# Performance work log

Hardware: AMD Instinct MI355X
Metric: run time of the kernel (lower is better)

## Reference

```python
import jax, jax.numpy as jnp
import numpy as np
from jax import lax

OBS_LEN = 8
PRED_LEN = 12
BATCH = 131072
EMB = 128
HID = 128


def _lstm_cell(h, c, x, Wih, Whh, b):
    # PyTorch LSTM gate order: i, f, g, o
    z = x @ Wih + h @ Whh + b  # (B, 4H)
    i, f, g, o = jnp.split(z, 4, axis=-1)
    c_new = jax.nn.sigmoid(f) * c + jax.nn.sigmoid(i) * jnp.tanh(g)
    h_new = jax.nn.sigmoid(o) * jnp.tanh(c_new)
    return h_new, c_new


def setup_inputs() -> dict:
    key = jax.random.key(0)
    ks = jax.random.split(key, 8)
    p = lambda k, s: jax.random.normal(k, s, dtype=jnp.float32) * 0.1
    return {
        "obs_traj": jax.random.normal(ks[0], (OBS_LEN, BATCH, 2), dtype=jnp.float32),
        # encoder input embedding (Linear 2 -> EMB)
        "We": p(ks[1], (2, EMB)), "be": jnp.zeros((EMB,), jnp.float32),
        # encoder LSTM
        "Wih_e": p(ks[2], (EMB, 4 * HID)), "Whh_e": p(ks[3], (HID, 4 * HID)),
        "b_e": jnp.zeros((4 * HID,), jnp.float32),
        # decoder input embedding (Linear 2 -> EMB)
        "Wd": p(ks[4], (2, EMB)), "bd": jnp.zeros((EMB,), jnp.float32),
        # decoder LSTM
        "Wih_d": p(ks[5], (EMB, 4 * HID)), "Whh_d": p(ks[6], (HID, 4 * HID)),
        "b_d": jnp.zeros((4 * HID,), jnp.float32),
        # hidden2pos (Linear HID -> 2)
        "Wo": p(ks[7], (HID, 2)), "bo": jnp.zeros((2,), jnp.float32),
        "pred_len": PRED_LEN,
    }


def reference(obs_traj, We, be, Wih_e, Whh_e, b_e, Wd, bd, Wih_d, Whh_d, b_d, Wo, bo, pred_len):
    B = obs_traj.shape[1]
    H = Whh_e.shape[0]
    dt = obs_traj.dtype

    # ---- Encoder: embed positions, run LSTM over obs_len ----
    emb = obs_traj @ We + be  # (obs_len, B, EMB)
    h0 = jnp.zeros((B, H), dt)
    c0 = jnp.zeros((B, H), dt)

    def enc_step(carry, x_t):
        h, c = carry
        h, c = _lstm_cell(h, c, x_t, Wih_e, Whh_e, b_e)
        return (h, c), None

    (h_enc, _), _ = lax.scan(enc_step, (h0, c0), emb)

    # ---- Decoder: state = (h_final, zeros); first pos directly from h_final ----
    pos0 = h_enc @ Wo + bo  # (B, 2)
    h_d = h_enc
    c_d = jnp.zeros_like(h_enc)

    def dec_step(carry, _):
        h, c, pos = carry
        x = pos @ Wd + bd  # embed previous predicted position
        h, c = _lstm_cell(h, c, x, Wih_d, Whh_d, b_d)
        pos_new = h @ Wo + bo
        return (h, c, pos_new), pos_new

    _, rest = lax.scan(dec_step, (h_d, c_d, pos0), None, length=pred_len - 1)
    pred_traj = jnp.concatenate([pos0[None], rest], axis=0)  # (pred_len, B, 2)
    return pred_traj
```

## Files before the change

### kernel.cpp

```cpp
#include <hip/hip_runtime.h>


#define OBS_LEN 8
#define PRED_LEN 12
#define BATCH 131072
#define HID 128
#define NZ 512
#define KWT 128
#define XK 32
#define A2S 40

typedef float f32x4 __attribute__((ext_vector_type(4)));
typedef float f32x2 __attribute__((ext_vector_type(2)));
typedef unsigned short u16x8 __attribute__((ext_vector_type(8)));
typedef __bf16 bf16x8 __attribute__((ext_vector_type(8)));

#define K2F 1.4426950408889634f

static __device__ __forceinline__ unsigned short cvt1(float f) {
  __bf16 b = (__bf16)f;
  return __builtin_bit_cast(unsigned short, b);
}
static __device__ __forceinline__ float bf2f(unsigned short h) {
  return __uint_as_float(((unsigned int)h) << 16);
}

__global__ void prep_weights(const float* __restrict__ We,   const float* __restrict__ be,
                             const float* __restrict__ Wih_e,const float* __restrict__ Whh_e,
                             const float* __restrict__ b_e,
                             const float* __restrict__ Wd,   const float* __restrict__ bd,
                             const float* __restrict__ Wih_d,const float* __restrict__ Whh_d,
                             const float* __restrict__ b_d,
                             const float* __restrict__ Wo,   const float* __restrict__ bo,
                             unsigned short* __restrict__ wt_enc,
                             unsigned short* __restrict__ wt_dec,
                             unsigned short* __restrict__ xw_enc,
                             unsigned short* __restrict__ xw_dec) {
  const int c = blockIdx.x & (NZ - 1);
  const bool dec = blockIdx.x >= NZ;
  const int cg = c >> 6, gate = (c >> 4) & 3, cl = c & 15;
  const int unit = cg * 16 + cl;
  const int n = gate * HID + unit;
  const float s = (gate == 2) ? (-2.f * K2F) : (-K2F);

  const float* Whh = dec ? Whh_d : Whh_e;
  const float* Wih = dec ? Wih_d : Wih_e;
  const float* Wem = dec ? Wd : We;
  const float* bem = dec ? bd : be;
  const float* bl  = dec ? b_d : b_e;
  unsigned short* wt = dec ? wt_dec : wt_enc;
  unsigned short* xw = dec ? xw_dec : xw_enc;

  float wx = 0.f, wy = 0.f;
  for (int e = 0; e < HID; ++e) {
    wx += Wem[e] * Wih[e * NZ + n];
    wy += Wem[HID + e] * Wih[e * NZ + n];
  }
  for (int k = threadIdx.x; k < KWT; k += 64) {
    float v = Whh[k * NZ + n];
    if (dec) v += Wo[k * 2] * wx + Wo[k * 2 + 1] * wy;
    wt[c * KWT + k] = cvt1(s * v);
  }
  if (threadIdx.x == 0) {
    float bb = bl[n];
    for (int e = 0; e < HID; ++e) bb += bem[e] * Wih[e * NZ + n];
    if (dec) bb += bo[0] * wx + bo[1] * wy;
    unsigned short* xr = xw + c * XK;
    for (int k = 5; k < XK; ++k) xr[k] = 0;
    if (dec) {
      xr[0] = 0; xr[1] = 0; xr[2] = cvt1(s * bb); xr[3] = 0; xr[4] = 0;
    } else {
      xr[0] = cvt1(s * wx); xr[1] = cvt1(s * wy); xr[2] = cvt1(s * bb);
      xr[3] = xr[0]; xr[4] = xr[1];
    }
  }
}


#define MFMA(A, B, C)                                                          \
  __builtin_amdgcn_mfma_f32_16x16x32_bf16(                                     \
      __builtin_bit_cast(bf16x8, (A)), __builtin_bit_cast(bf16x8, (B)), (C),   \
      0, 0, 0)

#define EXP4(D, S)                                                             \
  { f32x4 _s = (S);                                                            \
    D[0] = __builtin_amdgcn_exp2f(_s[0]); D[1] = __builtin_amdgcn_exp2f(_s[1]);\
    D[2] = __builtin_amdgcn_exp2f(_s[2]); D[3] = __builtin_amdgcn_exp2f(_s[3]); }
#define RCP4(D, S)                                                             \
  { f32x4 _r = (S);                                                            \
    D[0] = __builtin_amdgcn_rcpf(_r[0]); D[1] = __builtin_amdgcn_rcpf(_r[1]);  \
    D[2] = __builtin_amdgcn_rcpf(_r[2]); D[3] = __builtin_amdgcn_rcpf(_r[3]); }

#define LOADW(WT, XW)                                                          \
  { _Pragma("unroll")                                                          \
    for (int kc = 0; kc < 4; ++kc) {                                           \
      _Pragma("unroll")                                                        \
      for (int g = 0; g < 4; ++g)                                              \
        bfr[kc][g] =                                                           \
            *(const u16x8*)&(WT)[(cg * 64 + g * 16 + l15) * KWT + kc * 32 +    \
                                 l4 * 8];                                      \
    }                                                                          \
    _Pragma("unroll")                                                          \
    for (int g = 0; g < 4; ++g)                                                \
      xfr[g] = *(const u16x8*)&(XW)[(cg * 64 + g * 16 + l15) * XK + l4 * 8]; }

#define MMX(ACC, X)                                                            \
  { u16x8 mm_a2a = *(const u16x8*)&A2[(X)*32 * A2S + l15 * A2S + l4 * 8];      \
    u16x8 mm_a2b =                                                             \
        *(const u16x8*)&A2[(X)*32 * A2S + (16 + l15) * A2S + l4 * 8];          \
    _Pragma("unroll")                                                          \
    for (int g = 0; g < 4; ++g) {                                              \
      ACC[0][g] = MFMA(mm_a2a, xfr[g], ZROV);                                  \
      ACC[1][g] = MFMA(mm_a2b, xfr[g], ZROV);                                  \
    }                                                                          \
    _Pragma("unroll")                                                          \
    for (int kc = 0; kc < 4; ++kc) {                                           \
      const int mm_g = (((kc * 4 + l4) ^ l15) << 3);                           \
      u16x8 mm_a0 = *(const u16x8*)&hL[(X)*4096 + l15 * 128 + mm_g];           \
      u16x8 mm_a1 = *(const u16x8*)&hL[(X)*4096 + (16 + l15) * 128 + mm_g];    \
      _Pragma("unroll")                                                        \
      for (int g = 0; g < 4; ++g) {                                            \
        ACC[0][g] = MFMA(mm_a0, bfr[kc][g], ACC[0][g]);                        \
        ACC[1][g] = MFMA(mm_a1, bfr[kc][g], ACC[1][g]);                        \
      } } }

#define GATEC(ACC, CRR, X)                                                     \
  { _Pragma("unroll")                                                          \
    for (int m = 0; m < 2; ++m) {                                              \
      f32x4 g_eB, g_eA, g_eG, g_eO;                                            \
      EXP4(g_eB, ACC[m][0]) EXP4(g_eA, ACC[m][1])                              \
      EXP4(g_eG, ACC[m][2]) EXP4(g_eO, ACC[m][3])                              \
      f32x4 g_a1 = 1.f + g_eA, g_b1 = 1.f + g_eB, g_g1 = 1.f + g_eG;           \
      f32x4 g_bg = g_b1 * g_g1;                                                \
      f32x4 g_rd; RCP4(g_rd, g_a1 * g_bg)                                      \
      f32x4 g_cv = (CRR[m] * g_bg + (1.f - g_eG) * g_a1) * g_rd;               \
      CRR[m] = g_cv;                                                           \
      f32x4 g_eC; EXP4(g_eC, g_cv * (-2.f * K2F))                              \
      f32x4 g_rh; RCP4(g_rh, (1.f + g_eO) * (1.f + g_eC))                      \
      f32x4 g_hv = (1.f - g_eC) * g_rh;                                        \
      const int g_R0 = 16 * m + l4 * 4;                                        \
      _Pragma("unroll")                                                        \
      for (int r = 0; r < 4; ++r)                                              \
        hL[(X)*4096 + (g_R0 + r) * 128 +                                       \
           ((uh ^ ((g_R0 + r) & 15)) << 3) + ul] = cvt1(g_hv[r]);              \
    } }

#define POSC(S, X)                                                             \
  { const int pp_r = tid >> 4, pp_q = tid & 15;                                \
    u16x8 pp_h = *(const u16x8*)&hL[(X)*4096 + pp_r * 128 +                    \
                                    ((pp_q ^ (pp_r & 15)) << 3)];              \
    const float* pp_w = WoL + pp_q * 16;                                       \
    f32x4 pp_w0 = *(const f32x4*)pp_w;                                         \
    f32x4 pp_w1 = *(const f32x4*)(pp_w + 4);                                   \
    f32x4 pp_w2 = *(const f32x4*)(pp_w + 8);                                   \
    f32x4 pp_w3 = *(const f32x4*)(pp_w + 12);                                  \
    f32x2 pp_s = (f32x2){0.f, 0.f};                                            \
    pp_s += bf2f(pp_h[0]) * (f32x2){pp_w0[0], pp_w0[1]};                       \
    pp_s += bf2f(pp_h[1]) * (f32x2){pp_w0[2], pp_w0[3]};                       \
    pp_s += bf2f(pp_h[2]) * (f32x2){pp_w1[0], pp_w1[1]};                       \
    pp_s += bf2f(pp_h[3]) * (f32x2){pp_w1[2], pp_w1[3]};                       \
    pp_s += bf2f(pp_h[4]) * (f32x2){pp_w2[0], pp_w2[1]};                       \
    pp_s += bf2f(pp_h[5]) * (f32x2){pp_w2[2], pp_w2[3]};                       \
    pp_s += bf2f(pp_h[6]) * (f32x2){pp_w3[0], pp_w3[1]};                       \
    pp_s += bf2f(pp_h[7]) * (f32x2){pp_w3[2], pp_w3[3]};                       \
    pp_s[0] += __shfl_xor(pp_s[0], 1); pp_s[1] += __shfl_xor(pp_s[1], 1);      \
    pp_s[0] += __shfl_xor(pp_s[0], 2); pp_s[1] += __shfl_xor(pp_s[1], 2);      \
    pp_s[0] += __shfl_xor(pp_s[0], 4); pp_s[1] += __shfl_xor(pp_s[1], 4);      \
    pp_s[0] += __shfl_xor(pp_s[0], 8); pp_s[1] += __shfl_xor(pp_s[1], 8);      \
    if (pp_q == 0) {                                                           \
      float2 pp_o; pp_o.x = pp_s[0] + bo0; pp_o.y = pp_s[1] + bo1;             \
      ((float2*)out)[(size_t)(S)*BATCH + row0 + (X)*32 + pp_r] = pp_o;         \
    } }

#define STAGE_OBS_A2(T, X)                                                     \
  if (tid < 32) {                                                              \
    float2 so_p =                                                              \
        ((const float2*)obs)[(size_t)(T)*BATCH + row0 + (X)*32 + tid];         \
    unsigned short so_x = cvt1(so_p.x), so_y = cvt1(so_p.y);                   \
    unsigned short* so_r = &A2[(X)*32 * A2S + tid * A2S];                      \
    so_r[0] = so_x; so_r[1] = so_y; so_r[2] = 0x3F80u;                         \
    so_r[3] = cvt1(so_p.x - bf2f(so_x));                                       \
    so_r[4] = cvt1(so_p.y - bf2f(so_y));                                       \
  }

#define STAGE_DEC_A2(X)                                                        \
  if (tid < 32) {                                                              \
    unsigned short* sd_r = &A2[(X)*32 * A2S + tid * A2S];                      \
    sd_r[0] = 0; sd_r[1] = 0; sd_r[2] = 0x3F80u; sd_r[3] = 0; sd_r[4] = 0;     \
  }

__global__ __launch_bounds__(512, 2) void lstm_fused(
    const float* __restrict__ obs,
    const unsigned short* __restrict__ wt_enc,
    const unsigned short* __restrict__ wt_dec,
    const unsigned short* __restrict__ xw_enc,
    const unsigned short* __restrict__ xw_dec,
    const float* __restrict__ Wo, const float* __restrict__ bo,
    float* __restrict__ out) {
  __shared__ unsigned short hL[2 * 32 * 128];
  __shared__ unsigned short A2[2 * 32 * A2S];
  __shared__ float WoL[HID * 2];

  const int tid = threadIdx.x;
  const int lane = tid & 63;
  const int cg = tid >> 6;
  const int l15 = lane & 15;
  const int l4 = lane >> 4;
  const int row0 = blockIdx.x * 64;
  const int u = cg * 16 + l15, uh = u >> 3, ul = u & 7;
  const float bo0 = bo[0], bo1 = bo[1];
  const f32x4 ZROV = {0.f, 0.f, 0.f, 0.f};

  {
    u16x8 z8 = (u16x8){0, 0, 0, 0, 0, 0, 0, 0};
    *(u16x8*)&hL[tid * 8] = z8;
    *(u16x8*)&hL[4096 + tid * 8] = z8;
    unsigned short* az = &A2[tid * 5];
    az[0] = 0; az[1] = 0; az[2] = 0; az[3] = 0; az[4] = 0;
  }
  if (tid < HID) { WoL[tid * 2] = Wo[tid * 2]; WoL[tid * 2 + 1] = Wo[tid * 2 + 1]; }

  u16x8 bfr[4][4], xfr[4];
  LOADW(wt_enc, xw_enc);

  f32x4 accA[2][4], accB[2][4];
  f32x4 crrA[2], crrB[2];
  crrA[0] = crrA[1] = ZROV;
  crrB[0] = crrB[1] = ZROV;
  __syncthreads();

  STAGE_OBS_A2(0, 0)
  __syncthreads();

#pragma unroll 1
  for (int t = 0; t < OBS_LEN; ++t) {
    MMX(accA, 0)
    if (t > 0) { GATEC(accB, crrB, 1) }
    STAGE_OBS_A2(t, 1)
    __syncthreads();
    MMX(accB, 1)
    GATEC(accA, crrA, 0)
    if (t + 1 < OBS_LEN) { STAGE_OBS_A2(t + 1, 0) }
    else { STAGE_DEC_A2(0) }
    __syncthreads();
  }

  LOADW(wt_dec, xw_dec);
  crrA[0] = crrA[1] = ZROV;

  MMX(accA, 0)
  GATEC(accB, crrB, 1)
  POSC(0, 0)
  STAGE_DEC_A2(1)
  __syncthreads();
  crrB[0] = crrB[1] = ZROV;

  MMX(accB, 1)
  GATEC(accA, crrA, 0)
  POSC(0, 1)
  __syncthreads();

#pragma unroll 1
  for (int d = 2; d < PRED_LEN; ++d) {
    MMX(accA, 0)
    GATEC(accB, crrB, 1)
    POSC(d - 1, 0)
    __syncthreads();
    MMX(accB, 1)
    GATEC(accA, crrA, 0)
    POSC(d - 1, 1)
    __syncthreads();
  }

  GATEC(accB, crrB, 1)
  POSC(PRED_LEN - 1, 0)
  __syncthreads();
  POSC(PRED_LEN - 1, 1)
}

extern "C" void kernel_launch(void* const* d_in, const int* in_sizes, int n_in,
                              void* d_out, int out_size, void* d_ws, size_t ws_size,
                              hipStream_t stream) {
  const float* obs   = (const float*)d_in[0];
  const float* We    = (const float*)d_in[1];
  const float* be    = (const float*)d_in[2];
  const float* Wih_e = (const float*)d_in[3];
  const float* Whh_e = (const float*)d_in[4];
  const float* b_e   = (const float*)d_in[5];
  const float* Wd    = (const float*)d_in[6];
  const float* bd    = (const float*)d_in[7];
  const float* Wih_d = (const float*)d_in[8];
  const float* Whh_d = (const float*)d_in[9];
  const float* b_d   = (const float*)d_in[10];
  const float* Wo    = (const float*)d_in[11];
  const float* bo    = (const float*)d_in[12];
  float* out = (float*)d_out;

  unsigned short* wt_enc = (unsigned short*)d_ws;
  unsigned short* wt_dec = wt_enc + NZ * KWT;
  unsigned short* xw_enc = wt_dec + NZ * KWT;
  unsigned short* xw_dec = xw_enc + NZ * XK;

  hipLaunchKernelGGL(prep_weights, dim3(2 * NZ), dim3(64), 0, stream,
                     We, be, Wih_e, Whh_e, b_e, Wd, bd, Wih_d, Whh_d, b_d,
                     Wo, bo, wt_enc, wt_dec, xw_enc, xw_dec);
  hipLaunchKernelGGL(lstm_fused, dim3(BATCH / 64), dim3(512), 0, stream,
                     obs, wt_enc, wt_dec, xw_enc, xw_dec, Wo, bo, out);
}
```

Before: 521.1 us.

## Drop decoder bias MFMAs, init accumulators from fp32 bias, keep Wo in registers

In the decoder the input-projection MFMA against a constant bias row is replaced by initialising the accumulators directly from an fp32 per-column bias precomputed in the prep kernel. This removes eight MFMAs and the A2 loads per half-step, and keeps the bias in fp32 instead of bf16. Wo is now held in per-thread registers rather than staged in LDS, and the matmul for each half is moved after the gate and staging work so it sits just before the barrier. Register pressure rises, with 16 Wo floats plus 4 bias values live per thread under a 512x2 launch bound.

```diff
diff --git a/kernel.cpp b/kernel.cpp
--- a/kernel.cpp
+++ b/kernel.cpp
@@ -35,7 +35,7 @@
                              unsigned short* __restrict__ wt_enc,
                              unsigned short* __restrict__ wt_dec,
                              unsigned short* __restrict__ xw_enc,
-                             unsigned short* __restrict__ xw_dec) {
+                             float* __restrict__ auxf_dec) {
   const int c = blockIdx.x & (NZ - 1);
   const bool dec = blockIdx.x >= NZ;
   const int cg = c >> 6, gate = (c >> 4) & 3, cl = c & 15;
@@ -49,7 +49,6 @@
   const float* bem = dec ? bd : be;
   const float* bl  = dec ? b_d : b_e;
   unsigned short* wt = dec ? wt_dec : wt_enc;
-  unsigned short* xw = dec ? xw_dec : xw_enc;
 
   float wx = 0.f, wy = 0.f;
   for (int e = 0; e < HID; ++e) {
@@ -64,12 +63,12 @@
   if (threadIdx.x == 0) {
     float bb = bl[n];
     for (int e = 0; e < HID; ++e) bb += bem[e] * Wih[e * NZ + n];
-    if (dec) bb += bo[0] * wx + bo[1] * wy;
-    unsigned short* xr = xw + c * XK;
-    for (int k = 5; k < XK; ++k) xr[k] = 0;
     if (dec) {
-      xr[0] = 0; xr[1] = 0; xr[2] = cvt1(s * bb); xr[3] = 0; xr[4] = 0;
+      bb += bo[0] * wx + bo[1] * wy;
+      auxf_dec[c] = s * bb;
     } else {
+      unsigned short* xr = xw_enc + c * XK;
+      for (int k = 5; k < XK; ++k) xr[k] = 0;
       xr[0] = cvt1(s * wx); xr[1] = cvt1(s * wy); xr[2] = cvt1(s * bb);
       xr[3] = xr[0]; xr[4] = xr[1];
     }
@@ -91,7 +90,7 @@
     D[0] = __builtin_amdgcn_rcpf(_r[0]); D[1] = __builtin_amdgcn_rcpf(_r[1]);  \
     D[2] = __builtin_amdgcn_rcpf(_r[2]); D[3] = __builtin_amdgcn_rcpf(_r[3]); }
 
-#define LOADW(WT, XW)                                                          \
+#define LOADW_BF(WT)                                                           \
   { _Pragma("unroll")                                                          \
     for (int kc = 0; kc < 4; ++kc) {                                           \
       _Pragma("unroll")                                                        \
@@ -99,21 +98,10 @@
         bfr[kc][g] =                                                           \
             *(const u16x8*)&(WT)[(cg * 64 + g * 16 + l15) * KWT + kc * 32 +    \
                                  l4 * 8];                                      \
-    }                                                                          \
-    _Pragma("unroll")                                                          \
-    for (int g = 0; g < 4; ++g)                                                \
-      xfr[g] = *(const u16x8*)&(XW)[(cg * 64 + g * 16 + l15) * XK + l4 * 8]; }
-
-#define MMX(ACC, X)                                                            \
-  { u16x8 mm_a2a = *(const u16x8*)&A2[(X)*32 * A2S + l15 * A2S + l4 * 8];      \
-    u16x8 mm_a2b =                                                             \
-        *(const u16x8*)&A2[(X)*32 * A2S + (16 + l15) * A2S + l4 * 8];          \
-    _Pragma("unroll")                                                          \
-    for (int g = 0; g < 4; ++g) {                                              \
-      ACC[0][g] = MFMA(mm_a2a, xfr[g], ZROV);                                  \
-      ACC[1][g] = MFMA(mm_a2b, xfr[g], ZROV);                                  \
-    }                                                                          \
-    _Pragma("unroll")                                                          \
+    } }
+
+#define MMH(ACC, X)                                                            \
+  { _Pragma("unroll")                                                          \
     for (int kc = 0; kc < 4; ++kc) {                                           \
       const int mm_g = (((kc * 4 + l4) ^ l15) << 3);                           \
       u16x8 mm_a0 = *(const u16x8*)&hL[(X)*4096 + l15 * 128 + mm_g];           \
@@ -123,6 +111,25 @@
         ACC[0][g] = MFMA(mm_a0, bfr[kc][g], ACC[0][g]);                        \
         ACC[1][g] = MFMA(mm_a1, bfr[kc][g], ACC[1][g]);                        \
       } } }
+
+#define MMXE(ACC, X)                                                           \
+  { u16x8 mm_a2a = *(const u16x8*)&A2[(X)*32 * A2S + l15 * A2S + l4 * 8];      \
+    u16x8 mm_a2b =                                                             \
+        *(const u16x8*)&A2[(X)*32 * A2S + (16 + l15) * A2S + l4 * 8];          \
+    _Pragma("unroll")                                                          \
+    for (int g = 0; g < 4; ++g) {                                              \
+      ACC[0][g] = MFMA(mm_a2a, xfr[g], ZROV);                                  \
+      ACC[1][g] = MFMA(mm_a2b, xfr[g], ZROV);                                  \
+    }                                                                          \
+    MMH(ACC, X) }
+
+#define INITD(ACC)                                                             \
+  { _Pragma("unroll")                                                          \
+    for (int m = 0; m < 2; ++m) {                                              \
+      _Pragma("unroll")                                                        \
+      for (int g = 0; g < 4; ++g)                                              \
+        ACC[m][g] = (f32x4){bbD[g], bbD[g], bbD[g], bbD[g]};                   \
+    } }
 
 #define GATEC(ACC, CRR, X)                                                     \
   { _Pragma("unroll")                                                          \
@@ -146,28 +153,23 @@
     } }
 
 #define POSC(S, X)                                                             \
-  { const int pp_r = tid >> 4, pp_q = tid & 15;                                \
+  { const int pp_r = tid >> 4;                                                 \
     u16x8 pp_h = *(const u16x8*)&hL[(X)*4096 + pp_r * 128 +                    \
-                                    ((pp_q ^ (pp_r & 15)) << 3)];              \
-    const float* pp_w = WoL + pp_q * 16;                                       \
-    f32x4 pp_w0 = *(const f32x4*)pp_w;                                         \
-    f32x4 pp_w1 = *(const f32x4*)(pp_w + 4);                                   \
-    f32x4 pp_w2 = *(const f32x4*)(pp_w + 8);                                   \
-    f32x4 pp_w3 = *(const f32x4*)(pp_w + 12);                                  \
+                                    ((pq ^ (pp_r & 15)) << 3)];                \
     f32x2 pp_s = (f32x2){0.f, 0.f};                                            \
-    pp_s += bf2f(pp_h[0]) * (f32x2){pp_w0[0], pp_w0[1]};                       \
-    pp_s += bf2f(pp_h[1]) * (f32x2){pp_w0[2], pp_w0[3]};                       \
-    pp_s += bf2f(pp_h[2]) * (f32x2){pp_w1[0], pp_w1[1]};                       \
-    pp_s += bf2f(pp_h[3]) * (f32x2){pp_w1[2], pp_w1[3]};                       \
-    pp_s += bf2f(pp_h[4]) * (f32x2){pp_w2[0], pp_w2[1]};                       \
-    pp_s += bf2f(pp_h[5]) * (f32x2){pp_w2[2], pp_w2[3]};                       \
-    pp_s += bf2f(pp_h[6]) * (f32x2){pp_w3[0], pp_w3[1]};                       \
-    pp_s += bf2f(pp_h[7]) * (f32x2){pp_w3[2], pp_w3[3]};                       \
+    pp_s += bf2f(pp_h[0]) * (f32x2){wo0[0], wo0[1]};                           \
+    pp_s += bf2f(pp_h[1]) * (f32x2){wo0[2], wo0[3]};                           \
+    pp_s += bf2f(pp_h[2]) * (f32x2){wo1[0], wo1[1]};                           \
+    pp_s += bf2f(pp_h[3]) * (f32x2){wo1[2], wo1[3]};                           \
+    pp_s += bf2f(pp_h[4]) * (f32x2){wo2[0], wo2[1]};                           \
+    pp_s += bf2f(pp_h[5]) * (f32x2){wo2[2], wo2[3]};                           \
+    pp_s += bf2f(pp_h[6]) * (f32x2){wo3[0], wo3[1]};                           \
+    pp_s += bf2f(pp_h[7]) * (f32x2){wo3[2], wo3[3]};                           \
     pp_s[0] += __shfl_xor(pp_s[0], 1); pp_s[1] += __shfl_xor(pp_s[1], 1);      \
     pp_s[0] += __shfl_xor(pp_s[0], 2); pp_s[1] += __shfl_xor(pp_s[1], 2);      \
     pp_s[0] += __shfl_xor(pp_s[0], 4); pp_s[1] += __shfl_xor(pp_s[1], 4);      \
     pp_s[0] += __shfl_xor(pp_s[0], 8); pp_s[1] += __shfl_xor(pp_s[1], 8);      \
-    if (pp_q == 0) {                                                           \
+    if (pq == 0) {                                                             \
       float2 pp_o; pp_o.x = pp_s[0] + bo0; pp_o.y = pp_s[1] + bo1;             \
       ((float2*)out)[(size_t)(S)*BATCH + row0 + (X)*32 + pp_r] = pp_o;         \
     } }
@@ -183,29 +185,23 @@
     so_r[4] = cvt1(so_p.y - bf2f(so_y));                                       \
   }
 
-#define STAGE_DEC_A2(X)                                                        \
-  if (tid < 32) {                                                              \
-    unsigned short* sd_r = &A2[(X)*32 * A2S + tid * A2S];                      \
-    sd_r[0] = 0; sd_r[1] = 0; sd_r[2] = 0x3F80u; sd_r[3] = 0; sd_r[4] = 0;     \
-  }
-
 __global__ __launch_bounds__(512, 2) void lstm_fused(
     const float* __restrict__ obs,
     const unsigned short* __restrict__ wt_enc,
     const unsigned short* __restrict__ wt_dec,
     const unsigned short* __restrict__ xw_enc,
-    const unsigned short* __restrict__ xw_dec,
+    const float* __restrict__ auxf_dec,
     const float* __restrict__ Wo, const float* __restrict__ bo,
     float* __restrict__ out) {
   __shared__ unsigned short hL[2 * 32 * 128];
   __shared__ unsigned short A2[2 * 32 * A2S];
-  __shared__ float WoL[HID * 2];
 
   const int tid = threadIdx.x;
   const int lane = tid & 63;
   const int cg = tid >> 6;
   const int l15 = lane & 15;
   const int l4 = lane >> 4;
+  const int pq = tid & 15;
   const int row0 = blockIdx.x * 64;
   const int u = cg * 16 + l15, uh = u >> 3, ul = u & 7;
   const float bo0 = bo[0], bo1 = bo[1];
@@ -218,10 +214,17 @@
     unsigned short* az = &A2[tid * 5];
     az[0] = 0; az[1] = 0; az[2] = 0; az[3] = 0; az[4] = 0;
   }
-  if (tid < HID) { WoL[tid * 2] = Wo[tid * 2]; WoL[tid * 2 + 1] = Wo[tid * 2 + 1]; }
+  const float* wop = Wo + pq * 16;
+  const f32x4 wo0 = *(const f32x4*)wop;
+  const f32x4 wo1 = *(const f32x4*)(wop + 4);
+  const f32x4 wo2 = *(const f32x4*)(wop + 8);
+  const f32x4 wo3 = *(const f32x4*)(wop + 12);
 
   u16x8 bfr[4][4], xfr[4];
-  LOADW(wt_enc, xw_enc);
+  LOADW_BF(wt_enc);
+#pragma unroll
+  for (int g = 0; g < 4; ++g)
+    xfr[g] = *(const u16x8*)&xw_enc[(cg * 64 + g * 16 + l15) * XK + l4 * 8];
 
   f32x4 accA[2][4], accB[2][4];
   f32x4 crrA[2], crrB[2];
@@ -234,41 +237,46 @@
 
 #pragma unroll 1
   for (int t = 0; t < OBS_LEN; ++t) {
-    MMX(accA, 0)
     if (t > 0) { GATEC(accB, crrB, 1) }
     STAGE_OBS_A2(t, 1)
+    MMXE(accA, 0)
     __syncthreads();
-    MMX(accB, 1)
     GATEC(accA, crrA, 0)
     if (t + 1 < OBS_LEN) { STAGE_OBS_A2(t + 1, 0) }
-    else { STAGE_DEC_A2(0) }
+    MMXE(accB, 1)
     __syncthreads();
   }
 
-  LOADW(wt_dec, xw_dec);
+  LOADW_BF(wt_dec);
+  float bbD[4];
+#pragma unroll
+  for (int g = 0; g < 4; ++g) bbD[g] = auxf_dec[cg * 64 + g * 16 + l15];
   crrA[0] = crrA[1] = ZROV;
 
-  MMX(accA, 0)
   GATEC(accB, crrB, 1)
   POSC(0, 0)
-  STAGE_DEC_A2(1)
+  INITD(accA)
+  MMH(accA, 0)
   __syncthreads();
   crrB[0] = crrB[1] = ZROV;
 
-  MMX(accB, 1)
   GATEC(accA, crrA, 0)
   POSC(0, 1)
+  INITD(accB)
+  MMH(accB, 1)
   __syncthreads();
 
 #pragma unroll 1
   for (int d = 2; d < PRED_LEN; ++d) {
-    MMX(accA, 0)
     GATEC(accB, crrB, 1)
     POSC(d - 1, 0)
+    INITD(accA)
+    MMH(accA, 0)
     __syncthreads();
-    MMX(accB, 1)
     GATEC(accA, crrA, 0)
     POSC(d - 1, 1)
+    INITD(accB)
+    MMH(accB, 1)
     __syncthreads();
   }
 
@@ -299,11 +307,11 @@
   unsigned short* wt_enc = (unsigned short*)d_ws;
   unsigned short* wt_dec = wt_enc + NZ * KWT;
   unsigned short* xw_enc = wt_dec + NZ * KWT;
-  unsigned short* xw_dec = xw_enc + NZ * XK;
+  float* auxf_dec = (float*)(xw_enc + NZ * XK);
 
   hipLaunchKernelGGL(prep_weights, dim3(2 * NZ), dim3(64), 0, stream,
                      We, be, Wih_e, Whh_e, b_e, Wd, bd, Wih_d, Whh_d, b_d,
-                     Wo, bo, wt_enc, wt_dec, xw_enc, xw_dec);
+                     Wo, bo, wt_enc, wt_dec, xw_enc, auxf_dec);
   hipLaunchKernelGGL(lstm_fused, dim3(BATCH / 64), dim3(512), 0, stream,
-                     obs, wt_enc, wt_dec, xw_enc, xw_dec, Wo, bo, out);
-}
+                     obs, wt_enc, wt_dec, xw_enc, auxf_dec, Wo, bo, out);
+}
```

After: 502.2 us. 3.6% less time.
